# Performance work log

Hardware: AMD Instinct MI355X
Metric: run time of the kernel (lower is better)

Reference implementation:

```python
import jax, jax.numpy as jnp
import numpy as np
import math

D_MODEL = 1024
N_HEADS = 16
D_HEAD = D_MODEL // N_HEADS
B, L, S = 2, 2048, 2048


def setup_inputs() -> dict:
    key = jax.random.key(0)
    ks = jax.random.split(key, 20)
    f32 = jnp.float32
    def lin(k):
        kw, kb = jax.random.split(k)
        W = jax.random.normal(kw, (D_MODEL, D_MODEL), f32) * 0.02
        b = jax.random.normal(kb, (D_MODEL,), f32) * 0.02
        return W, b
    Wq, bq = lin(ks[0]); Wk, bk = lin(ks[1]); Wv, bv = lin(ks[2])
    Wqb, bqb = lin(ks[3]); Wkg, bkg = lin(ks[4]); Wvb, bvb = lin(ks[5])
    Wo, bo = lin(ks[6])
    return {
        "queries": jax.random.normal(ks[7], (B, L, D_MODEL), f32),
        "keys": jax.random.normal(ks[8], (B, S, D_MODEL), f32),
        "values": jax.random.normal(ks[9], (B, S, D_MODEL), f32),
        "attn_mask": jax.random.randint(ks[10], (B, 1, L, S), 0, 2).astype(bool),
        "context": jax.random.normal(ks[11], (B, L, D_MODEL), f32),
        "Wq": Wq, "bq": bq, "Wk": Wk, "bk": bk, "Wv": Wv, "bv": bv,
        "Wqb": Wqb, "bqb": bqb, "Wkg": Wkg, "bkg": bkg, "Wvb": Wvb, "bvb": bvb,
        "Wo": Wo, "bo": bo,
    }


def reference(queries, keys, values, attn_mask, context,
              Wq, bq, Wk, bk, Wv, bv, Wqb, bqb, Wkg, bkg, Wvb, bvb, Wo, bo):
    B_, L_, _ = queries.shape
    S_ = keys.shape[1]
    H, dk = N_HEADS, D_HEAD
    # projections (Linear: x @ W + b), reshaped to [B, T, H, dk]
    Q = (queries @ Wq + bq).reshape(B_, L_, H, dk)
    K = (keys @ Wk + bk).reshape(B_, S_, H, dk)
    V = (values @ Wv + bv).reshape(B_, S_, H, dk)
    # context-based bias / gate
    Q = Q + (context @ Wqb + bqb).reshape(B_, L_, H, dk)
    K = K * jax.nn.sigmoid((context @ Wkg + bkg).reshape(B_, S_, H, dk))
    V = V + (context @ Wvb + bvb).reshape(B_, S_, H, dk)
    # scaled dot-product attention, [B, H, L, S]
    scores = jnp.einsum('blhd,bshd->bhls', Q, K) / math.sqrt(dk)
    scores = jnp.where(attn_mask, jnp.asarray(-1e9, scores.dtype), scores)
    attn_weights = jax.nn.softmax(scores, axis=-1)
    # dropout is identity in eval mode
    out = jnp.einsum('bhls,bshd->blhd', attn_weights, V).reshape(B_, L_, H * dk)
    return (out @ Wo + bo, attn_weights)
```

## Files before the change

### kernel.cpp

```cpp
#include <hip/hip_runtime.h>

typedef __attribute__((ext_vector_type(8))) short  s16x8;
typedef __attribute__((ext_vector_type(8))) unsigned short u16x8;
typedef __attribute__((ext_vector_type(4))) float  f32x4;

#define D_MODEL 1024
#define N_HEADS 16
#define D_HEAD  64
#define BATCH   2
#define SEQ     2048
#define M_TOK   4096

#define OFF_XQ  0u
#define OFF_XK  4194304u
#define OFF_XV  8388608u
#define OFF_XC  12582912u
#define OFF_WT  16777216u
#define OFF_QH  24117248u
#define OFF_KH  28311552u
#define OFF_VH  32505856u
#define OFF_OH  36700160u

__device__ __forceinline__ unsigned short f2bf(float f) {
    unsigned int u = __builtin_bit_cast(unsigned int, f);
    u += 0x7FFFu + ((u >> 16) & 1u);
    return (unsigned short)(u >> 16);
}

__device__ __forceinline__ unsigned int pk2bf(float a, float b) {
    return (unsigned int)f2bf(a) | ((unsigned int)f2bf(b) << 16);
}

__device__ __forceinline__ void gload16(const void* g, void* l) {
    __builtin_amdgcn_global_load_lds(
        (const __attribute__((address_space(1))) unsigned int*)g,
        (__attribute__((address_space(3))) unsigned int*)l, 16, 0, 0);
}

__device__ __forceinline__ f32x4 mfma16(s16x8 a, s16x8 b, f32x4 c) {
    return __builtin_amdgcn_mfma_f32_16x16x32_bf16(a, b, c, 0, 0, 0);
}

__device__ __forceinline__ f32x4 zero4() {
    f32x4 z; z[0] = 0.f; z[1] = 0.f; z[2] = 0.f; z[3] = 0.f; return z;
}

struct P4 { const float* p[4]; };
struct P7 { const float* p[7]; };

__global__ __launch_bounds__(256) void cvt4(P4 srcs, unsigned short* dst) {
    const int a = blockIdx.y;
    const float* s = srcs.p[a];
    unsigned short* d = dst + ((size_t)a << 22);
    const size_t i = (((size_t)blockIdx.x << 8) + threadIdx.x) << 3;
    const float4 v0 = *(const float4*)(s + i);
    const float4 v1 = *(const float4*)(s + i + 4);
    u16x8 o;
    o[0] = f2bf(v0.x); o[1] = f2bf(v0.y); o[2] = f2bf(v0.z); o[3] = f2bf(v0.w);
    o[4] = f2bf(v1.x); o[5] = f2bf(v1.y); o[6] = f2bf(v1.z); o[7] = f2bf(v1.w);
    *(u16x8*)(d + i) = o;
}

__global__ __launch_bounds__(256) void wtr(P7 srcs, unsigned short* dst) {
    const int z = blockIdx.z;
    const float* W = srcs.p[z];
    unsigned short* Wt = dst + ((size_t)z << 20);
    __shared__ float T[32][33];
    const int t = threadIdx.x;
    const int r = t >> 3, c4 = (t & 7) << 2;
    const int kt = blockIdx.y << 5, nt = blockIdx.x << 5;
    const float4 v = *(const float4*)(W + ((size_t)(kt + r) << 10) + nt + c4);
    T[r][c4] = v.x; T[r][c4 + 1] = v.y; T[r][c4 + 2] = v.z; T[r][c4 + 3] = v.w;
    __syncthreads();
    ushort4 o;
    o.x = f2bf(T[c4 + 0][r]); o.y = f2bf(T[c4 + 1][r]);
    o.z = f2bf(T[c4 + 2][r]); o.w = f2bf(T[c4 + 3][r]);
    *(ushort4*)(Wt + ((size_t)(nt + r) << 10) + kt + c4) = o;
}

__global__ __launch_bounds__(256) void vtr(const unsigned short* __restrict__ Vh,
                                           unsigned short* __restrict__ VhT) {
    __shared__ unsigned short T[64][72];
    const int bh = blockIdx.y, s0 = blockIdx.x << 6;
    const unsigned short* src = Vh + ((size_t)bh * 2048 + s0) * 64;
    unsigned short* dst = VhT + (size_t)bh * 64 * 2048 + s0;
    const int t = threadIdx.x;
    const int r = t >> 3, c0 = (t & 7) << 3;
    #pragma unroll
    for (int it = 0; it < 2; ++it) {
        const int rr = it * 32 + r;
        const u16x8 v = *(const u16x8*)(src + (size_t)rr * 64 + c0);
        #pragma unroll
        for (int i = 0; i < 8; ++i) T[c0 + i][rr] = v[i];
    }
    __syncthreads();
    #pragma unroll
    for (int it = 0; it < 2; ++it) {
        const int rr = it * 32 + r;
        u16x8 o;
        #pragma unroll
        for (int i = 0; i < 8; ++i) o[i] = T[rr][c0 + i];
        *(u16x8*)(dst + (size_t)rr * 2048 + c0) = o;
    }
}

__global__ __launch_bounds__(256) void mpack(const unsigned char* __restrict__ maskp,
                                             unsigned long long* __restrict__ mb) {
    const unsigned int probe = ((const unsigned int*)maskp)[threadIdx.x & 63];
    const bool isInt = __all(probe <= 1u);
    const size_t i = ((size_t)blockIdx.x << 8) + threadIdx.x;
    bool v;
    if (isInt) v = ((const int*)maskp)[i] != 0;
    else       v = maskp[i] != 0;
    const unsigned long long bal = __ballot(v);
    if ((threadIdx.x & 63) == 0) mb[i >> 6] = bal;
}

struct ProjDesc {
    const unsigned short *A0, *A1, *B0, *B1;
    const float *b0, *b1;
    unsigned short* dst;
    float scale;
    int gate;
};
struct ProjArgs { ProjDesc d[3]; };

__global__ __launch_bounds__(256) void proj_all(ProjArgs pa) {
    const ProjDesc P = pa.d[blockIdx.z];
    __shared__ unsigned short Al[128 * 32];
    __shared__ unsigned short Bl[64 * 32];
    const int tid = threadIdx.x;
    const int wid = tid >> 6, lane = tid & 63;
    const int lo = lane & 15, hi = lane >> 4;
    const int wr = wid >> 1, wc = wid & 1;
    const int m0 = blockIdx.y << 7, n0 = blockIdx.x << 6;

    auto stage = [&](const unsigned short* As, const unsigned short* Bs, int k0) {
        #pragma unroll
        for (int it = 0; it < 2; ++it) {
            const int c = it * 256 + tid;
            const int r = c >> 2, j = c & 3;
            gload16(As + ((size_t)(m0 + r) << 10) + k0 + j * 8, Al + c * 8);
        }
        const int rb = tid >> 2, jb = tid & 3;
        gload16(Bs + ((size_t)(n0 + rb) << 10) + k0 + jb * 8, Bl + tid * 8);
    };
    auto compute = [&](f32x4 (&acc)[4][2]) {
        s16x8 af[4], bfr[2];
        #pragma unroll
        for (int mi = 0; mi < 4; ++mi)
            af[mi] = *(const s16x8*)&Al[(wr * 64 + mi * 16 + lo) * 32 + hi * 8];
        #pragma unroll
        for (int ni = 0; ni < 2; ++ni)
            bfr[ni] = *(const s16x8*)&Bl[(wc * 32 + ni * 16 + lo) * 32 + hi * 8];
        __builtin_amdgcn_s_setprio(1);
        #pragma unroll
        for (int mi = 0; mi < 4; ++mi)
            #pragma unroll
            for (int ni = 0; ni < 2; ++ni)
                acc[mi][ni] = mfma16(af[mi], bfr[ni], acc[mi][ni]);
        __builtin_amdgcn_s_setprio(0);
    };

    if (P.gate) {
        f32x4 acc0[4][2], acc1[4][2];
        #pragma unroll
        for (int i = 0; i < 4; ++i)
            #pragma unroll
            for (int j = 0; j < 2; ++j) { acc0[i][j] = zero4(); acc1[i][j] = zero4(); }
        for (int kt = 0; kt < 32; ++kt) {
            __syncthreads();
            stage(P.A0, P.B0, kt << 5);
            __syncthreads();
            compute(acc0);
        }
        for (int kt = 0; kt < 32; ++kt) {
            __syncthreads();
            stage(P.A1, P.B1, kt << 5);
            __syncthreads();
            compute(acc1);
        }
        #pragma unroll
        for (int mi = 0; mi < 4; ++mi)
            #pragma unroll
            for (int ni = 0; ni < 2; ++ni) {
                const int n = n0 + wc * 32 + ni * 16 + lo;
                const float b0 = P.b0[n], b1 = P.b1[n];
                const int h = n >> 6, d = n & 63;
                #pragma unroll
                for (int reg = 0; reg < 4; ++reg) {
                    const int m = m0 + wr * 64 + mi * 16 + hi * 4 + reg;
                    const int b = m >> 11, t = m & 2047;
                    const float kv = acc0[mi][ni][reg] + b0;
                    const float gv = acc1[mi][ni][reg] + b1;
                    const float sg = 1.0f / (1.0f + __expf(-gv));
                    P.dst[((size_t)((b * 16 + h) * 2048 + t) << 6) + d] = f2bf(kv * sg);
                }
            }
    } else {
        f32x4 acc[4][2];
        #pragma unroll
        for (int i = 0; i < 4; ++i)
            #pragma unroll
            for (int j = 0; j < 2; ++j) acc[i][j] = zero4();
        for (int kt = 0; kt < 64; ++kt) {
            const unsigned short* As = (kt < 32) ? P.A0 : P.A1;
            const unsigned short* Bs = (kt < 32) ? P.B0 : P.B1;
            __syncthreads();
            stage(As, Bs, (kt & 31) << 5);
            __syncthreads();
            compute(acc);
        }
        #pragma unroll
        for (int mi = 0; mi < 4; ++mi)
            #pragma unroll
            for (int ni = 0; ni < 2; ++ni) {
                const int n = n0 + wc * 32 + ni * 16 + lo;
                const float bsum = P.b0[n] + P.b1[n];
                const int h = n >> 6, d = n & 63;
                #pragma unroll
                for (int reg = 0; reg < 4; ++reg) {
                    const int m = m0 + wr * 64 + mi * 16 + hi * 4 + reg;
                    const int b = m >> 11, t = m & 2047;
                    P.dst[((size_t)((b * 16 + h) * 2048 + t) << 6) + d] =
                        f2bf((acc[mi][ni][reg] + bsum) * P.scale);
                }
            }
    }
}

__global__ __launch_bounds__(256) void gemm_out(
    const unsigned short* __restrict__ A, const unsigned short* __restrict__ Bt,
    const float* __restrict__ bias, float* __restrict__ out)
{
    __shared__ unsigned short Al[128 * 32];
    __shared__ unsigned short Bl[64 * 32];
    const int tid = threadIdx.x;
    const int wid = tid >> 6, lane = tid & 63;
    const int lo = lane & 15, hi = lane >> 4;
    const int wr = wid >> 1, wc = wid & 1;
    const int m0 = blockIdx.y << 7, n0 = blockIdx.x << 6;

    f32x4 acc[4][2];
    #pragma unroll
    for (int i = 0; i < 4; ++i)
        #pragma unroll
        for (int j = 0; j < 2; ++j) acc[i][j] = zero4();

    for (int kt = 0; kt < 32; ++kt) {
        const int k0 = kt << 5;
        __syncthreads();
        #pragma unroll
        for (int it = 0; it < 2; ++it) {
            const int c = it * 256 + tid;
            const int r = c >> 2, j = c & 3;
            gload16(A + ((size_t)(m0 + r) << 10) + k0 + j * 8, Al + c * 8);
        }
        {
            const int rb = tid >> 2, jb = tid & 3;
            gload16(Bt + ((size_t)(n0 + rb) << 10) + k0 + jb * 8, Bl + tid * 8);
        }
        __syncthreads();
        s16x8 af[4], bfr[2];
        #pragma unroll
        for (int mi = 0; mi < 4; ++mi)
            af[mi] = *(const s16x8*)&Al[(wr * 64 + mi * 16 + lo) * 32 + hi * 8];
        #pragma unroll
        for (int ni = 0; ni < 2; ++ni)
            bfr[ni] = *(const s16x8*)&Bl[(wc * 32 + ni * 16 + lo) * 32 + hi * 8];
        __builtin_amdgcn_s_setprio(1);
        #pragma unroll
        for (int mi = 0; mi < 4; ++mi)
            #pragma unroll
            for (int ni = 0; ni < 2; ++ni)
                acc[mi][ni] = mfma16(af[mi], bfr[ni], acc[mi][ni]);
        __builtin_amdgcn_s_setprio(0);
    }

    #pragma unroll
    for (int mi = 0; mi < 4; ++mi)
        #pragma unroll
        for (int ni = 0; ni < 2; ++ni) {
            const int n = n0 + wc * 32 + ni * 16 + lo;
            const float bb = bias[n];
            #pragma unroll
            for (int reg = 0; reg < 4; ++reg) {
                const int m = m0 + wr * 64 + mi * 16 + hi * 4 + reg;
                out[((size_t)m << 10) + n] = acc[mi][ni][reg] + bb;
            }
        }
}

__global__ __launch_bounds__(256, 4) void attn_fused(
    const unsigned short* __restrict__ Qh, const unsigned short* __restrict__ Kh,
    const unsigned short* __restrict__ VhT, const unsigned long long* __restrict__ mbits,
    float* __restrict__ attnW, unsigned short* __restrict__ Oh)
{
    __shared__ unsigned short Ks[2][4096];
    __shared__ unsigned short Vs[2][4096];
    __shared__ unsigned short Ps[4][1024];

    const int tid = threadIdx.x;
    const int wid = tid >> 6, lane = tid & 63;
    const int lo = lane & 15, hi = lane >> 4;

    const int wg = blockIdx.x;
    const int gid = (wg & 7) * 128 + (wg >> 3);
    const int bh = gid >> 5, lt = gid & 31;
    const int b = bh >> 4, hh = bh & 15;
    const int l0 = lt << 6;

    const unsigned short* Qp = Qh + ((size_t)bh * 2048 + l0) * 64;
    const unsigned short* Kp = Kh + (size_t)bh * 2048 * 64;
    const unsigned short* Vp = VhT + (size_t)bh * 64 * 2048;

    const int q = wid * 16 + lo;
    float* Wrow = attnW + ((size_t)bh * 2048 + l0 + q) * 2048 + hi * 4;
    const unsigned long long* mq = mbits + ((size_t)b * 2048 + l0 + q) * 32;

    s16x8 qf[2];
    {
        const unsigned short* qr = Qp + (size_t)q * 64 + hi * 8;
        qf[0] = *(const s16x8*)qr;
        qf[1] = *(const s16x8*)(qr + 32);
    }

    auto stageK = [&](int st, int bufi) {
        const unsigned short* src = Kp + (size_t)(st << 6) * 64;
        #pragma unroll
        for (int it = 0; it < 2; ++it) {
            const int c = it * 256 + tid;
            const int r = c >> 3, j = c & 7;
            gload16(src + (size_t)r * 64 + ((j ^ (r & 7)) << 3), &Ks[bufi][c * 8]);
        }
    };
    auto stageV = [&](int st, int bufi) {
        const unsigned short* src = Vp + (st << 6);
        #pragma unroll
        for (int it = 0; it < 2; ++it) {
            const int c = it * 256 + tid;
            const int r = c >> 3, j = c & 7;
            gload16(src + (size_t)r * 2048 + ((j ^ (r & 7)) << 3), &Vs[bufi][c * 8]);
        }
    };

    float lsum = 0.f;
    stageK(0, 0);
    __syncthreads();
    for (int st = 0; st < 32; ++st) {
        const int cur = st & 1;
        if (st < 31) stageK(st + 1, cur ^ 1);

        const unsigned long long mrow = mq[st] >> (hi * 4);
        f32x4 sf[4];
        #pragma unroll
        for (int ni = 0; ni < 4; ++ni) sf[ni] = zero4();
        __builtin_amdgcn_s_setprio(1);
        #pragma unroll
        for (int ks = 0; ks < 2; ++ks)
            #pragma unroll
            for (int ni = 0; ni < 4; ++ni) {
                const int rn = ni * 16 + lo;
                const s16x8 kf = *(const s16x8*)&Ks[cur][rn * 64 + (((hi + ks * 4) ^ (rn & 7)) << 3)];
                sf[ni] = mfma16(kf, qf[ks], sf[ni]);
            }
        __builtin_amdgcn_s_setprio(0);
        #pragma unroll
        for (int ni = 0; ni < 4; ++ni)
            #pragma unroll
            for (int reg = 0; reg < 4; ++reg) {
                const unsigned int bit = (unsigned int)(mrow >> (ni * 16 + reg)) & 1u;
                lsum += bit ? 0.f : __expf(sf[ni][reg]);
            }
        __syncthreads();
    }
    lsum += __shfl_xor(lsum, 16);
    lsum += __shfl_xor(lsum, 32);
    const float il = 1.0f / lsum;

    f32x4 oacc[4];
    #pragma unroll
    for (int nd = 0; nd < 4; ++nd) oacc[nd] = zero4();

    stageK(0, 0);
    stageV(0, 0);
    __syncthreads();
    for (int st = 0; st < 32; ++st) {
        const int cur = st & 1;
        if (st < 31) { stageK(st + 1, cur ^ 1); stageV(st + 1, cur ^ 1); }

        const unsigned long long mrow = mq[st] >> (hi * 4);
        f32x4 sf[4];
        #pragma unroll
        for (int ni = 0; ni < 4; ++ni) sf[ni] = zero4();
        __builtin_amdgcn_s_setprio(1);
        #pragma unroll
        for (int ks = 0; ks < 2; ++ks)
            #pragma unroll
            for (int ni = 0; ni < 4; ++ni) {
                const int rn = ni * 16 + lo;
                const s16x8 kf = *(const s16x8*)&Ks[cur][rn * 64 + (((hi + ks * 4) ^ (rn & 7)) << 3)];
                sf[ni] = mfma16(kf, qf[ks], sf[ni]);
            }
        __builtin_amdgcn_s_setprio(0);

        #pragma unroll
        for (int ni = 0; ni < 4; ++ni) {
            f32x4 wv;
            #pragma unroll
            for (int reg = 0; reg < 4; ++reg) {
                const unsigned int bit = (unsigned int)(mrow >> (ni * 16 + reg)) & 1u;
                const float e = bit ? 0.f : __expf(sf[ni][reg]);
                wv[reg] = e * il;
            }
            __builtin_nontemporal_store(wv, (f32x4*)(Wrow + (size_t)st * 64 + ni * 16));
            const unsigned int p01 = pk2bf(wv[0], wv[1]);
            const unsigned int p23 = pk2bf(wv[2], wv[3]);
            *(uint2*)((char*)&Ps[wid][0] + lo * 128 + ((ni * 32 + hi * 8) ^ ((lo & 7) << 4))) =
                make_uint2(p01, p23);
        }

        __builtin_amdgcn_s_setprio(1);
        #pragma unroll
        for (int ks = 0; ks < 2; ++ks) {
            const s16x8 pf = *(const s16x8*)((const char*)&Ps[wid][0] +
                lo * 128 + ((ks * 64 + hi * 16) ^ ((lo & 7) << 4)));
            #pragma unroll
            for (int nd = 0; nd < 4; ++nd) {
                const int rv = nd * 16 + lo;
                const s16x8 vf = *(const s16x8*)&Vs[cur][rv * 64 + (((hi + ks * 4) ^ (rv & 7)) << 3)];
                oacc[nd] = mfma16(pf, vf, oacc[nd]);
            }
        }
        __builtin_amdgcn_s_setprio(0);
        __syncthreads();
    }

    #pragma unroll
    for (int nd = 0; nd < 4; ++nd)
        #pragma unroll
        for (int reg = 0; reg < 4; ++reg) {
            const int rl = wid * 16 + hi * 4 + reg;
            const int d = nd * 16 + lo;
            Oh[((size_t)(b * 2048 + l0 + rl) << 10) + hh * 64 + d] = f2bf(oacc[nd][reg]);
        }
}

extern "C" void kernel_launch(void* const* d_in, const int* in_sizes, int n_in,
                              void* d_out, int out_size, void* d_ws, size_t ws_size,
                              hipStream_t stream) {
    const float* queries = (const float*)d_in[0];
    const float* keys    = (const float*)d_in[1];
    const float* values  = (const float*)d_in[2];
    const unsigned char* mask = (const unsigned char*)d_in[3];
    const float* context = (const float*)d_in[4];
    const float* Wq  = (const float*)d_in[5];  const float* bq  = (const float*)d_in[6];
    const float* Wk  = (const float*)d_in[7];  const float* bk  = (const float*)d_in[8];
    const float* Wv  = (const float*)d_in[9];  const float* bv  = (const float*)d_in[10];
    const float* Wqb = (const float*)d_in[11]; const float* bqb = (const float*)d_in[12];
    const float* Wkg = (const float*)d_in[13]; const float* bkg = (const float*)d_in[14];
    const float* Wvb = (const float*)d_in[15]; const float* bvb = (const float*)d_in[16];
    const float* Wo  = (const float*)d_in[17]; const float* bo  = (const float*)d_in[18];

    unsigned short* ws = (unsigned short*)d_ws;
    unsigned short* xq = ws + OFF_XQ;
    unsigned short* xk = ws + OFF_XK;
    unsigned short* xv = ws + OFF_XV;
    unsigned short* xc = ws + OFF_XC;
    unsigned short* wt = ws + OFF_WT;
    unsigned short* Qh = ws + OFF_QH;
    unsigned short* Kh = ws + OFF_KH;
    unsigned short* Vh = ws + OFF_VH;
    unsigned short* Oh = ws + OFF_OH;
    unsigned short* VhT = ws + OFF_XQ;
    unsigned long long* mbits = (unsigned long long*)(ws + OFF_XV);

    float* out0  = (float*)d_out;
    float* attnW = out0 + 4194304;

    P4 acts; acts.p[0] = queries; acts.p[1] = keys; acts.p[2] = values; acts.p[3] = context;
    cvt4<<<dim3(2048, 4), 256, 0, stream>>>(acts, xq);

    P7 wts; wts.p[0] = Wq; wts.p[1] = Wqb; wts.p[2] = Wk; wts.p[3] = Wkg;
    wts.p[4] = Wv; wts.p[5] = Wvb; wts.p[6] = Wo;
    wtr<<<dim3(32, 32, 7), 256, 0, stream>>>(wts, wt);

    ProjArgs pa;
    pa.d[0] = { xq, xc, wt, wt + 1048576u, bq, bqb, Qh, 0.125f, 0 };
    pa.d[1] = { xv, xc, wt + 4u * 1048576u, wt + 5u * 1048576u, bv, bvb, Vh, 1.0f, 0 };
    pa.d[2] = { xk, xc, wt + 2u * 1048576u, wt + 3u * 1048576u, bk, bkg, Kh, 1.0f, 1 };
    proj_all<<<dim3(16, 32, 3), 256, 0, stream>>>(pa);

    vtr<<<dim3(32, 32), 256, 0, stream>>>(Vh, VhT);
    mpack<<<dim3(32768), 256, 0, stream>>>(mask, mbits);

    attn_fused<<<dim3(1024), 256, 0, stream>>>(Qh, Kh, VhT, mbits, attnW, Oh);

    gemm_out<<<dim3(16, 32), 256, 0, stream>>>(Oh, wt + 6u * 1048576u, bo, out0);
}
```

Baseline: 379.1 us.

## Double-buffer GEMM LDS staging, use exp2 with folded log2e, hardware bf16 pack

The projection and output GEMMs now use two LDS buffers and prefetch the next K tile while computing the current one, which removes one barrier per iteration and overlaps global loads with MFMA work. The gated and non-gated projection paths are merged into a single loop with two accumulators. The attention softmax switches from __expf to exp2f, with log2(e) folded into the Q scale (0.125*1.4427). P is packed to bf16 with the hardware v_cvt_pk_bf16_f32 instruction instead of manual rounding. LDS use doubles, and the merged projection loop holds two accumulator sets in every case, which may raise register pressure.

```diff
diff --git a/kernel.cpp b/kernel.cpp
--- a/kernel.cpp
+++ b/kernel.cpp
@@ -27,8 +27,10 @@
     return (unsigned short)(u >> 16);
 }
 
-__device__ __forceinline__ unsigned int pk2bf(float a, float b) {
-    return (unsigned int)f2bf(a) | ((unsigned int)f2bf(b) << 16);
+__device__ __forceinline__ unsigned int cvtpk(float a, float b) {
+    unsigned int r;
+    asm("v_cvt_pk_bf16_f32 %0, %1, %2" : "=v"(r) : "v"(a), "v"(b));
+    return r;
 }
 
 __device__ __forceinline__ void gload16(const void* g, void* l) {
@@ -127,147 +129,131 @@
 
 __global__ __launch_bounds__(256) void proj_all(ProjArgs pa) {
     const ProjDesc P = pa.d[blockIdx.z];
-    __shared__ unsigned short Al[128 * 32];
-    __shared__ unsigned short Bl[64 * 32];
+    __shared__ unsigned short Al[2][128 * 32];
+    __shared__ unsigned short Bl[2][64 * 32];
     const int tid = threadIdx.x;
     const int wid = tid >> 6, lane = tid & 63;
     const int lo = lane & 15, hi = lane >> 4;
     const int wr = wid >> 1, wc = wid & 1;
     const int m0 = blockIdx.y << 7, n0 = blockIdx.x << 6;
 
-    auto stage = [&](const unsigned short* As, const unsigned short* Bs, int k0) {
+    auto stageT = [&](int t) {
+        const int bufi = t & 1;
+        const unsigned short* As = (t < 32) ? P.A0 : P.A1;
+        const unsigned short* Bs = (t < 32) ? P.B0 : P.B1;
+        const int k0 = (t & 31) << 5;
         #pragma unroll
         for (int it = 0; it < 2; ++it) {
             const int c = it * 256 + tid;
             const int r = c >> 2, j = c & 3;
-            gload16(As + ((size_t)(m0 + r) << 10) + k0 + j * 8, Al + c * 8);
+            gload16(As + ((size_t)(m0 + r) << 10) + k0 + j * 8, &Al[bufi][c * 8]);
         }
         const int rb = tid >> 2, jb = tid & 3;
-        gload16(Bs + ((size_t)(n0 + rb) << 10) + k0 + jb * 8, Bl + tid * 8);
+        gload16(Bs + ((size_t)(n0 + rb) << 10) + k0 + jb * 8, &Bl[bufi][tid * 8]);
     };
-    auto compute = [&](f32x4 (&acc)[4][2]) {
+
+    f32x4 acc0[4][2], acc1[4][2];
+    #pragma unroll
+    for (int i = 0; i < 4; ++i)
+        #pragma unroll
+        for (int j = 0; j < 2; ++j) { acc0[i][j] = zero4(); acc1[i][j] = zero4(); }
+
+    stageT(0);
+    for (int t = 0; t < 64; ++t) {
+        __syncthreads();
+        if (t < 63) stageT(t + 1);
+        const int bufi = t & 1;
         s16x8 af[4], bfr[2];
         #pragma unroll
         for (int mi = 0; mi < 4; ++mi)
-            af[mi] = *(const s16x8*)&Al[(wr * 64 + mi * 16 + lo) * 32 + hi * 8];
+            af[mi] = *(const s16x8*)&Al[bufi][(wr * 64 + mi * 16 + lo) * 32 + hi * 8];
         #pragma unroll
         for (int ni = 0; ni < 2; ++ni)
-            bfr[ni] = *(const s16x8*)&Bl[(wc * 32 + ni * 16 + lo) * 32 + hi * 8];
+            bfr[ni] = *(const s16x8*)&Bl[bufi][(wc * 32 + ni * 16 + lo) * 32 + hi * 8];
         __builtin_amdgcn_s_setprio(1);
-        #pragma unroll
-        for (int mi = 0; mi < 4; ++mi)
-            #pragma unroll
-            for (int ni = 0; ni < 2; ++ni)
-                acc[mi][ni] = mfma16(af[mi], bfr[ni], acc[mi][ni]);
+        if (t < 32) {
+            #pragma unroll
+            for (int mi = 0; mi < 4; ++mi)
+                #pragma unroll
+                for (int ni = 0; ni < 2; ++ni)
+                    acc0[mi][ni] = mfma16(af[mi], bfr[ni], acc0[mi][ni]);
+        } else {
+            #pragma unroll
+            for (int mi = 0; mi < 4; ++mi)
+                #pragma unroll
+                for (int ni = 0; ni < 2; ++ni)
+                    acc1[mi][ni] = mfma16(af[mi], bfr[ni], acc1[mi][ni]);
+        }
         __builtin_amdgcn_s_setprio(0);
-    };
-
-    if (P.gate) {
-        f32x4 acc0[4][2], acc1[4][2];
-        #pragma unroll
-        for (int i = 0; i < 4; ++i)
-            #pragma unroll
-            for (int j = 0; j < 2; ++j) { acc0[i][j] = zero4(); acc1[i][j] = zero4(); }
-        for (int kt = 0; kt < 32; ++kt) {
-            __syncthreads();
-            stage(P.A0, P.B0, kt << 5);
-            __syncthreads();
-            compute(acc0);
-        }
-        for (int kt = 0; kt < 32; ++kt) {
-            __syncthreads();
-            stage(P.A1, P.B1, kt << 5);
-            __syncthreads();
-            compute(acc1);
-        }
-        #pragma unroll
-        for (int mi = 0; mi < 4; ++mi)
-            #pragma unroll
-            for (int ni = 0; ni < 2; ++ni) {
-                const int n = n0 + wc * 32 + ni * 16 + lo;
-                const float b0 = P.b0[n], b1 = P.b1[n];
-                const int h = n >> 6, d = n & 63;
-                #pragma unroll
-                for (int reg = 0; reg < 4; ++reg) {
-                    const int m = m0 + wr * 64 + mi * 16 + hi * 4 + reg;
-                    const int b = m >> 11, t = m & 2047;
+    }
+
+    #pragma unroll
+    for (int mi = 0; mi < 4; ++mi)
+        #pragma unroll
+        for (int ni = 0; ni < 2; ++ni) {
+            const int n = n0 + wc * 32 + ni * 16 + lo;
+            const float b0 = P.b0[n], b1 = P.b1[n];
+            const int h = n >> 6, d = n & 63;
+            #pragma unroll
+            for (int reg = 0; reg < 4; ++reg) {
+                const int m = m0 + wr * 64 + mi * 16 + hi * 4 + reg;
+                const int b = m >> 11, t = m & 2047;
+                float val;
+                if (P.gate) {
                     const float kv = acc0[mi][ni][reg] + b0;
                     const float gv = acc1[mi][ni][reg] + b1;
-                    const float sg = 1.0f / (1.0f + __expf(-gv));
-                    P.dst[((size_t)((b * 16 + h) * 2048 + t) << 6) + d] = f2bf(kv * sg);
+                    val = kv * (1.0f / (1.0f + __expf(-gv)));
+                } else {
+                    val = (acc0[mi][ni][reg] + acc1[mi][ni][reg] + b0 + b1) * P.scale;
                 }
-            }
-    } else {
-        f32x4 acc[4][2];
-        #pragma unroll
-        for (int i = 0; i < 4; ++i)
-            #pragma unroll
-            for (int j = 0; j < 2; ++j) acc[i][j] = zero4();
-        for (int kt = 0; kt < 64; ++kt) {
-            const unsigned short* As = (kt < 32) ? P.A0 : P.A1;
-            const unsigned short* Bs = (kt < 32) ? P.B0 : P.B1;
-            __syncthreads();
-            stage(As, Bs, (kt & 31) << 5);
-            __syncthreads();
-            compute(acc);
-        }
-        #pragma unroll
-        for (int mi = 0; mi < 4; ++mi)
-            #pragma unroll
-            for (int ni = 0; ni < 2; ++ni) {
-                const int n = n0 + wc * 32 + ni * 16 + lo;
-                const float bsum = P.b0[n] + P.b1[n];
-                const int h = n >> 6, d = n & 63;
-                #pragma unroll
-                for (int reg = 0; reg < 4; ++reg) {
-                    const int m = m0 + wr * 64 + mi * 16 + hi * 4 + reg;
-                    const int b = m >> 11, t = m & 2047;
-                    P.dst[((size_t)((b * 16 + h) * 2048 + t) << 6) + d] =
-                        f2bf((acc[mi][ni][reg] + bsum) * P.scale);
-                }
-            }
-    }
+                P.dst[((size_t)((b * 16 + h) * 2048 + t) << 6) + d] = f2bf(val);
+            }
+        }
 }
 
 __global__ __launch_bounds__(256) void gemm_out(
     const unsigned short* __restrict__ A, const unsigned short* __restrict__ Bt,
     const float* __restrict__ bias, float* __restrict__ out)
 {
-    __shared__ unsigned short Al[128 * 32];
-    __shared__ unsigned short Bl[64 * 32];
+    __shared__ unsigned short Al[2][128 * 32];
+    __shared__ unsigned short Bl[2][64 * 32];
     const int tid = threadIdx.x;
     const int wid = tid >> 6, lane = tid & 63;
     const int lo = lane & 15, hi = lane >> 4;
     const int wr = wid >> 1, wc = wid & 1;
     const int m0 = blockIdx.y << 7, n0 = blockIdx.x << 6;
 
-    f32x4 acc[4][2];
-    #pragma unroll
-    for (int i = 0; i < 4; ++i)
-        #pragma unroll
-        for (int j = 0; j < 2; ++j) acc[i][j] = zero4();
-
-    for (int kt = 0; kt < 32; ++kt) {
-        const int k0 = kt << 5;
-        __syncthreads();
+    auto stageT = [&](int t) {
+        const int bufi = t & 1;
+        const int k0 = t << 5;
         #pragma unroll
         for (int it = 0; it < 2; ++it) {
             const int c = it * 256 + tid;
             const int r = c >> 2, j = c & 3;
-            gload16(A + ((size_t)(m0 + r) << 10) + k0 + j * 8, Al + c * 8);
-        }
-        {
-            const int rb = tid >> 2, jb = tid & 3;
-            gload16(Bt + ((size_t)(n0 + rb) << 10) + k0 + jb * 8, Bl + tid * 8);
-        }
+            gload16(A + ((size_t)(m0 + r) << 10) + k0 + j * 8, &Al[bufi][c * 8]);
+        }
+        const int rb = tid >> 2, jb = tid & 3;
+        gload16(Bt + ((size_t)(n0 + rb) << 10) + k0 + jb * 8, &Bl[bufi][tid * 8]);
+    };
+
+    f32x4 acc[4][2];
+    #pragma unroll
+    for (int i = 0; i < 4; ++i)
+        #pragma unroll
+        for (int j = 0; j < 2; ++j) acc[i][j] = zero4();
+
+    stageT(0);
+    for (int t = 0; t < 32; ++t) {
         __syncthreads();
+        if (t < 31) stageT(t + 1);
+        const int bufi = t & 1;
         s16x8 af[4], bfr[2];
         #pragma unroll
         for (int mi = 0; mi < 4; ++mi)
-            af[mi] = *(const s16x8*)&Al[(wr * 64 + mi * 16 + lo) * 32 + hi * 8];
+            af[mi] = *(const s16x8*)&Al[bufi][(wr * 64 + mi * 16 + lo) * 32 + hi * 8];
         #pragma unroll
         for (int ni = 0; ni < 2; ++ni)
-            bfr[ni] = *(const s16x8*)&Bl[(wc * 32 + ni * 16 + lo) * 32 + hi * 8];
+            bfr[ni] = *(const s16x8*)&Bl[bufi][(wc * 32 + ni * 16 + lo) * 32 + hi * 8];
         __builtin_amdgcn_s_setprio(1);
         #pragma unroll
         for (int mi = 0; mi < 4; ++mi)
@@ -370,7 +356,7 @@
             #pragma unroll
             for (int reg = 0; reg < 4; ++reg) {
                 const unsigned int bit = (unsigned int)(mrow >> (ni * 16 + reg)) & 1u;
-                lsum += bit ? 0.f : __expf(sf[ni][reg]);
+                lsum += bit ? 0.f : exp2f(sf[ni][reg]);
             }
         __syncthreads();
     }
@@ -410,12 +396,12 @@
             #pragma unroll
             for (int reg = 0; reg < 4; ++reg) {
                 const unsigned int bit = (unsigned int)(mrow >> (ni * 16 + reg)) & 1u;
-                const float e = bit ? 0.f : __expf(sf[ni][reg]);
+                const float e = bit ? 0.f : exp2f(sf[ni][reg]);
                 wv[reg] = e * il;
             }
             __builtin_nontemporal_store(wv, (f32x4*)(Wrow + (size_t)st * 64 + ni * 16));
-            const unsigned int p01 = pk2bf(wv[0], wv[1]);
-            const unsigned int p23 = pk2bf(wv[2], wv[3]);
+            const unsigned int p01 = cvtpk(wv[0], wv[1]);
+            const unsigned int p23 = cvtpk(wv[2], wv[3]);
             *(uint2*)((char*)&Ps[wid][0] + lo * 128 + ((ni * 32 + hi * 8) ^ ((lo & 7) << 4))) =
                 make_uint2(p01, p23);
         }
@@ -486,7 +472,7 @@
     wtr<<<dim3(32, 32, 7), 256, 0, stream>>>(wts, wt);
 
     ProjArgs pa;
-    pa.d[0] = { xq, xc, wt, wt + 1048576u, bq, bqb, Qh, 0.125f, 0 };
+    pa.d[0] = { xq, xc, wt, wt + 1048576u, bq, bqb, Qh, 0.18033688f, 0 };
     pa.d[1] = { xv, xc, wt + 4u * 1048576u, wt + 5u * 1048576u, bv, bvb, Vh, 1.0f, 0 };
     pa.d[2] = { xk, xc, wt + 2u * 1048576u, wt + 3u * 1048576u, bk, bkg, Kh, 1.0f, 1 };
     proj_all<<<dim3(16, 32, 3), 256, 0, stream>>>(pa);
```

New measurement: 372.9 us. About the same (-1.6%).
